# Performance work log

Measured on AMD Instinct MI355X. Metric: run time of the kernel, lower is better.

Reference implementation:

```python
import jax, jax.numpy as jnp
import numpy as np

E = 8        # num_experts
D = 512      # embed_size
H = 8        # attention heads
HD = D // H  # head dim
B, S = 4, 1024


def setup_inputs() -> dict:
    key = jax.random.key(0)
    ks = jax.random.split(key, 16)
    sd = 0.02
    return {
        "x":  jax.random.normal(ks[0], (B, S, D), jnp.float32),
        # per-expert FFN params, stacked over expert dim
        "W1": jax.random.normal(ks[1], (E, D, 4 * D), jnp.float32) * sd,
        "b1": jnp.zeros((E, 4 * D), jnp.float32),
        "W2": jax.random.normal(ks[2], (E, 4 * D, D), jnp.float32) * sd,
        "b2": jnp.zeros((E, D), jnp.float32),
        # MultiheadAttention in_proj (split) and out_proj
        "Wq": jax.random.normal(ks[3], (D, D), jnp.float32) * sd,
        "bq": jnp.zeros((D,), jnp.float32),
        "Wk": jax.random.normal(ks[4], (D, D), jnp.float32) * sd,
        "bk": jnp.zeros((D,), jnp.float32),
        "Wv": jax.random.normal(ks[5], (D, D), jnp.float32) * sd,
        "bv": jnp.zeros((D,), jnp.float32),
        "Wo": jax.random.normal(ks[6], (D, D), jnp.float32) * sd,
        "bo": jnp.zeros((D,), jnp.float32),
        "expert_id": 3,
    }


def reference(x, W1, b1, W2, b2, Wq, bq, Wk, bk, Wv, bv, Wo, bo, expert_id):
    # --- batched per-expert FFN (fuses the Python loop over experts) ---
    # hidden: [B, E, S, 4D]
    hidden = jax.nn.relu(jnp.einsum('bsd,edf->besf', x, W1) + b1[None, :, None, :])
    eo = jnp.einsum('besf,efd->besd', hidden, W2) + b2[None, :, None, :]  # [B,E,S,D]
    eo = eo.transpose(0, 2, 1, 3)  # [B, S, E, D]

    Bs, Ss = x.shape[0], x.shape[1]
    a = eo.reshape(Bs * Ss, E, D)  # [N, E, D]; attention runs over the expert dim

    # --- MultiheadAttention (batch_first), torch semantics ---
    # NOTE: the original passes a FLOAT tril-of-ones attn_mask, which torch ADDS
    # to the scores (it does NOT mask with -inf). We reproduce that faithfully.
    q = (a @ Wq.T + bq).reshape(-1, E, H, HD).transpose(0, 2, 1, 3)  # [N,H,E,hd]
    k = (a @ Wk.T + bk).reshape(-1, E, H, HD).transpose(0, 2, 1, 3)
    v = (a @ Wv.T + bv).reshape(-1, E, H, HD).transpose(0, 2, 1, 3)

    mask = jnp.tril(jnp.ones((E, E), jnp.float32))  # additive float mask
    scores = jnp.einsum('nhed,nhfd->nhef', q, k) / jnp.sqrt(jnp.float32(HD))
    scores = scores + mask[None, None, :, :]
    attn = jax.nn.softmax(scores, axis=-1)
    ctx = jnp.einsum('nhef,nhfd->nhed', attn, v)           # [N,H,E,hd]
    ctx = ctx.transpose(0, 2, 1, 3).reshape(-1, E, D)       # [N,E,D]
    out = ctx @ Wo.T + bo                                   # [N,E,D]

    out = out.reshape(Bs, Ss, E, D)
    return out[:, :, expert_id, :]  # [B, S, D]
```

## Files before the change

### kernel.cpp

```cpp
#include <hip/hip_runtime.h>
#include <hip/hip_bf16.h>

typedef __hip_bfloat16 bf16;
typedef __attribute__((ext_vector_type(4))) float f32x4;
typedef __attribute__((ext_vector_type(8))) short s16x8;

#define N_TOK 4096
#define Dm    512
#define Fm    2048
#define Em    8

__device__ __forceinline__ float bf2f(bf16 v) { return __bfloat162float(v); }
__device__ __forceinline__ bf16  f2bf(float f) { return __float2bfloat16(f); }

#define GL16(g, l)                                                              \
  __builtin_amdgcn_global_load_lds(                                             \
      (const __attribute__((address_space(1))) void*)(g),                       \
      (__attribute__((address_space(3))) void*)(l), 16, 0, 0)

__global__ void cvt_f32_bf16(const float* __restrict__ in, bf16* __restrict__ out, int n4) {
  int i = blockIdx.x * 256 + threadIdx.x;
  if (i >= n4) return;
  float4 v = reinterpret_cast<const float4*>(in)[i];
  bf16 tmp[4] = {f2bf(v.x), f2bf(v.y), f2bf(v.z), f2bf(v.w)};
  __builtin_memcpy(out + (size_t)i * 4, tmp, 8);
}

__global__ void transpose_cvt(const float* __restrict__ in, bf16* __restrict__ out,
                              int R, int C, long inb, long outb) {
  in  += (long)blockIdx.z * inb;
  out += (long)blockIdx.z * outb;
  __shared__ float t[32][33];
  int tx = threadIdx.x & 31, ty = threadIdx.x >> 5;
  int c0 = blockIdx.x * 32, r0 = blockIdx.y * 32;
#pragma unroll
  for (int i = 0; i < 32; i += 8)
    t[ty + i][tx] = in[(long)(r0 + ty + i) * C + c0 + tx];
  __syncthreads();
#pragma unroll
  for (int i = 0; i < 32; i += 8)
    out[(long)(c0 + ty + i) * R + r0 + tx] = f2bf(t[tx][ty + i]);
}

template <bool RELU, bool OUT_BF16>
__global__ __launch_bounds__(256, 4) void gemm128(
    const bf16* __restrict__ A, const bf16* __restrict__ Bt, void* __restrict__ Cout,
    const float* __restrict__ bias, int K, int lda, int ldb, int ldc,
    long abs_, long bbs, long cbs, long biasbs,
    const int* __restrict__ eid, int eid_scale) {
  __shared__ bf16 As[128 * 64];
  __shared__ bf16 Bs[128 * 64];

  int e  = blockIdx.z;
  int bm = blockIdx.x * 128, bn = blockIdx.y * 128;

  A    += (long)e * abs_;
  Bt   += (long)e * bbs;
  bias += (long)e * biasbs;
  long coff = (long)e * cbs;
  if (eid) A += (long)(*eid) * eid_scale;

  int tid = threadIdx.x, wv = tid >> 6, lane = tid & 63;
  int wm = wv >> 1, wn = wv & 1;

  const bf16* Ab = A + (long)bm * lda;
  const bf16* Bb = Bt + (long)bn * ldb;

  f32x4 acc[4][4] = {};
  int la = lane & 15, q = lane >> 4;
  int srow_lo = lane >> 3;

  for (int k0 = 0; k0 < K; k0 += 64) {
    __syncthreads();
#pragma unroll
    for (int j = 0; j < 4; ++j) {
      int r = (wv * 4 + j) * 8 + srow_lo;
      int c = (lane & 7) ^ (r & 7);
      GL16(Ab + (long)r * lda + k0 + c * 8, As + (wv * 4 + j) * 512);
      GL16(Bb + (long)r * ldb + k0 + c * 8, Bs + (wv * 4 + j) * 512);
    }
    __syncthreads();

#pragma unroll
    for (int kk = 0; kk < 2; ++kk) {
      int ps = (kk * 4 + q) ^ (la & 7);
      s16x8 af[4], bfr[4];
#pragma unroll
      for (int m = 0; m < 4; ++m)
        af[m] = *reinterpret_cast<const s16x8*>(As + (wm * 64 + m * 16 + la) * 64 + ps * 8);
#pragma unroll
      for (int n = 0; n < 4; ++n)
        bfr[n] = *reinterpret_cast<const s16x8*>(Bs + (wn * 64 + n * 16 + la) * 64 + ps * 8);
#pragma unroll
      for (int m = 0; m < 4; ++m)
#pragma unroll
        for (int n = 0; n < 4; ++n)
          acc[m][n] = __builtin_amdgcn_mfma_f32_16x16x32_bf16(bfr[n], af[m], acc[m][n], 0, 0, 0);
    }
  }

#pragma unroll
  for (int m = 0; m < 4; ++m) {
    int gm = bm + wm * 64 + m * 16 + la;
#pragma unroll
    for (int n = 0; n < 4; ++n) {
      int gn = bn + wn * 64 + n * 16 + q * 4;
      float4 b4 = *reinterpret_cast<const float4*>(bias + gn);
      float v0 = acc[m][n][0] + b4.x, v1 = acc[m][n][1] + b4.y;
      float v2 = acc[m][n][2] + b4.z, v3 = acc[m][n][3] + b4.w;
      if (RELU) {
        v0 = fmaxf(v0, 0.f); v1 = fmaxf(v1, 0.f);
        v2 = fmaxf(v2, 0.f); v3 = fmaxf(v3, 0.f);
      }
      long idx = coff + (long)gm * ldc + gn;
      if (OUT_BF16) {
        bf16 tmp[4] = {f2bf(v0), f2bf(v1), f2bf(v2), f2bf(v3)};
        __builtin_memcpy((bf16*)Cout + idx, tmp, 8);
      } else {
        float tmp[4] = {v0, v1, v2, v3};
        __builtin_memcpy((float*)Cout + idx, tmp, 16);
      }
    }
  }
}

template <bool RELU, bool OUT_BF16>
__global__ __launch_bounds__(256, 2) void gemm_bt(
    const bf16* __restrict__ A, const bf16* __restrict__ Bt, void* __restrict__ Cout,
    const float* __restrict__ bias, int M, int N, int K, int lda, int ldb, int ldc,
    long abs_, long bbs, long cbs, long biasbs, const int* __restrict__ eid,
    int eid_scale) {
  int e = blockIdx.z;
  A    += (long)e * abs_;
  Bt   += (long)e * bbs;
  bias += (long)e * biasbs;
  long coff = (long)e * cbs;
  if (eid) A += (long)(*eid) * eid_scale;

  __shared__ bf16 As[128 * 32];
  __shared__ bf16 Bs[128 * 32];

  int tid = threadIdx.x;
  int wave = tid >> 6, lane = tid & 63;
  int wm = wave >> 1, wn = wave & 1;
  int bm = blockIdx.x * 128, bn = blockIdx.y * 128;

  int srow  = lane >> 2;
  int skoff = (lane & 3) * 8;

  f32x4 acc[4][4] = {};

  const bf16* Abase = A + (long)bm * lda;
  const bf16* Bbase = Bt + (long)bn * ldb;

  for (int k0 = 0; k0 < K; k0 += 32) {
    __syncthreads();
#pragma unroll
    for (int i = 0; i < 2; i++) {
      int r = wave * 32 + i * 16 + srow;
      GL16(Abase + (long)r * lda + k0 + skoff, As + (wave * 32 + i * 16) * 32);
      GL16(Bbase + (long)r * ldb + k0 + skoff, Bs + (wave * 32 + i * 16) * 32);
    }
    __syncthreads();

    s16x8 af[4], bfr[4];
#pragma unroll
    for (int m = 0; m < 4; m++)
      af[m] = *reinterpret_cast<const s16x8*>(As + (wm * 64 + m * 16 + (lane & 15)) * 32 +
                                              (lane >> 4) * 8);
#pragma unroll
    for (int n = 0; n < 4; n++)
      bfr[n] = *reinterpret_cast<const s16x8*>(Bs + (wn * 64 + n * 16 + (lane & 15)) * 32 +
                                               (lane >> 4) * 8);
#pragma unroll
    for (int m = 0; m < 4; m++)
#pragma unroll
      for (int n = 0; n < 4; n++)
        acc[m][n] = __builtin_amdgcn_mfma_f32_16x16x32_bf16(af[m], bfr[n], acc[m][n], 0, 0, 0);
  }

  int cr = (lane >> 4) * 4, cc = lane & 15;
#pragma unroll
  for (int m = 0; m < 4; m++) {
#pragma unroll
    for (int n = 0; n < 4; n++) {
      int col  = bn + wn * 64 + n * 16 + cc;
      float bv = bias ? bias[col] : 0.0f;
#pragma unroll
      for (int r = 0; r < 4; r++) {
        int row = bm + wm * 64 + m * 16 + cr + r;
        float v = acc[m][n][r] + bv;
        if (RELU) v = fmaxf(v, 0.0f);
        long idx = coff + (long)row * ldc + col;
        if (OUT_BF16)
          ((bf16*)Cout)[idx] = f2bf(v);
        else
          ((float*)Cout)[idx] = v;
      }
    }
  }
}

__global__ __launch_bounds__(256) void attn_kernel(const float* __restrict__ q,
                                                   const bf16* __restrict__ kv,
                                                   bf16* __restrict__ ctx,
                                                   const int* __restrict__ eid) {
  int wave = threadIdx.x >> 6, lane = threadIdx.x & 63;
  int n = blockIdx.x * 4 + wave;
  int h = lane >> 3, f = lane & 7;
  int e3 = *eid;
  const bf16* kvn = kv + (long)n * Em * (2 * Dm);
  const float* qh = q + (long)n * Dm + h * 64;
  const bf16* kf = kvn + f * (2 * Dm) + h * 64;
  float s = 0.f;
#pragma unroll
  for (int j = 0; j < 64; j++) s += qh[j] * bf2f(kf[j]);
  s *= 0.125f;
  s += (f <= e3) ? 1.0f : 0.0f;
  float mx = s;
#pragma unroll
  for (int d = 1; d < 8; d <<= 1) mx = fmaxf(mx, __shfl_xor(mx, d));
  float ex = expf(s - mx);
  float sm = ex;
#pragma unroll
  for (int d = 1; d < 8; d <<= 1) sm += __shfl_xor(sm, d);
  float at = ex / sm;
  int g = f;
  float acc[8] = {0, 0, 0, 0, 0, 0, 0, 0};
#pragma unroll
  for (int f2 = 0; f2 < 8; f2++) {
    float a = __shfl(at, (h << 3) | f2);
    const bf16* vf = kvn + f2 * (2 * Dm) + Dm + h * 64 + g * 8;
#pragma unroll
    for (int j = 0; j < 8; j++) acc[j] += a * bf2f(vf[j]);
  }
  bf16 tmp[8];
#pragma unroll
  for (int j = 0; j < 8; j++) tmp[j] = f2bf(acc[j]);
  __builtin_memcpy(ctx + (long)n * Dm + h * 64 + g * 8, tmp, 16);
}

extern "C" void kernel_launch(void* const* d_in, const int* in_sizes, int n_in,
                              void* d_out, int out_size, void* d_ws, size_t ws_size,
                              hipStream_t stream) {
  const float* x  = (const float*)d_in[0];
  const float* W1 = (const float*)d_in[1];
  const float* b1 = (const float*)d_in[2];
  const float* W2 = (const float*)d_in[3];
  const float* b2 = (const float*)d_in[4];
  const float* Wq = (const float*)d_in[5];
  const float* bq = (const float*)d_in[6];
  const float* Wk = (const float*)d_in[7];
  const float* bk = (const float*)d_in[8];
  const float* Wv = (const float*)d_in[9];
  const float* bv = (const float*)d_in[10];
  const float* Wo = (const float*)d_in[11];
  const float* bo = (const float*)d_in[12];
  const int* eid  = (const int*)d_in[13];

  char* w = (char*)d_ws;
  auto alloc = [&](size_t bytes) {
    char* p = w;
    w += (bytes + 255) & ~(size_t)255;
    return p;
  };
  bf16* xb   = (bf16*)alloc((size_t)N_TOK * Dm * 2);
  bf16* W1t  = (bf16*)alloc((size_t)Em * Fm * Dm * 2);
  bf16* W2t  = (bf16*)alloc((size_t)Em * Dm * Fm * 2);
  bf16* qw   = (bf16*)alloc((size_t)Dm * Dm * 2);
  bf16* kvw  = (bf16*)alloc((size_t)2 * Dm * Dm * 2);
  bf16* ow   = (bf16*)alloc((size_t)Dm * Dm * 2);
  float* bkv = (float*)alloc((size_t)2 * Dm * 4);
  bf16* hid  = (bf16*)alloc((size_t)Em * N_TOK * Fm * 2);
  bf16* eo   = (bf16*)alloc((size_t)N_TOK * Em * Dm * 2);
  bf16* kv   = (bf16*)hid;
  float* qb  = (float*)(hid + (size_t)N_TOK * Em * 2 * Dm);
  bf16* ctxb = (bf16*)(qb + (size_t)N_TOK * Dm);

  cvt_f32_bf16<<<(N_TOK * Dm / 4 + 255) / 256, 256, 0, stream>>>(x, xb, N_TOK * Dm / 4);
  transpose_cvt<<<dim3(Fm / 32, Dm / 32, Em), 256, 0, stream>>>(
      W1, W1t, Dm, Fm, (long)Dm * Fm, (long)Fm * Dm);
  transpose_cvt<<<dim3(Dm / 32, Fm / 32, Em), 256, 0, stream>>>(
      W2, W2t, Fm, Dm, (long)Fm * Dm, (long)Dm * Fm);
  int nw4 = Dm * Dm / 4;
  cvt_f32_bf16<<<(nw4 + 255) / 256, 256, 0, stream>>>(Wq, qw, nw4);
  cvt_f32_bf16<<<(nw4 + 255) / 256, 256, 0, stream>>>(Wk, kvw, nw4);
  cvt_f32_bf16<<<(nw4 + 255) / 256, 256, 0, stream>>>(Wv, kvw + (size_t)Dm * Dm, nw4);
  cvt_f32_bf16<<<(nw4 + 255) / 256, 256, 0, stream>>>(Wo, ow, nw4);
  hipMemcpyAsync(bkv, bk, Dm * sizeof(float), hipMemcpyDeviceToDevice, stream);
  hipMemcpyAsync(bkv + Dm, bv, Dm * sizeof(float), hipMemcpyDeviceToDevice, stream);

  gemm128<true, true><<<dim3(32, 16, Em), 256, 0, stream>>>(
      xb, W1t, hid, b1, Dm, Dm, Dm, Fm,
      0L, (long)Fm * Dm, (long)N_TOK * Fm, (long)Fm, nullptr, 0);
  gemm128<false, true><<<dim3(32, 4, Em), 256, 0, stream>>>(
      hid, W2t, eo, b2, Fm, Fm, Fm, Em * Dm,
      (long)N_TOK * Fm, (long)Dm * Fm, (long)Dm, (long)Dm, nullptr, 0);
  gemm128<false, true><<<dim3(256, 8, 1), 256, 0, stream>>>(
      eo, kvw, kv, bkv, Dm, Dm, Dm, 2 * Dm,
      0L, 0L, 0L, 0L, nullptr, 0);
  gemm_bt<false, false><<<dim3(N_TOK / 128, Dm / 128, 1), 256, 0, stream>>>(
      eo, qw, qb, bq, N_TOK, Dm, Dm, Em * Dm, Dm, Dm,
      0L, 0L, 0L, 0L, eid, Dm);
  attn_kernel<<<N_TOK / 4, 256, 0, stream>>>(qb, kv, ctxb, eid);
  gemm_bt<false, false><<<dim3(N_TOK / 128, Dm / 128, 1), 256, 0, stream>>>(
      ctxb, ow, (float*)d_out, bo, N_TOK, Dm, Dm, Dm, Dm, Dm,
      0L, 0L, 0L, 0L, nullptr, 0);
}
```

Before: 310.5 us.

## Replace LDS-staged GEMMs with direct global-to-register double-buffered MFMA GEMM

Drops the shared-memory staging (global_load_lds plus two barriers per k-step) and instead has each wave load its MFMA fragments straight from global memory into registers, using a two-stage register double buffer to overlap loads with MFMAs. The separate gemm_bt kernel is removed and all six GEMM launches go through the one new kernel. This removes LDS traffic and barriers, but gives up the sharing of data across waves, so each A/B fragment is fetched from global or L2 once per wave. The loads are 16-byte strided row reads that lean on cache hits.

```diff
diff --git a/kernel.cpp b/kernel.cpp
--- a/kernel.cpp
+++ b/kernel.cpp
@@ -12,11 +12,6 @@
 
 __device__ __forceinline__ float bf2f(bf16 v) { return __bfloat162float(v); }
 __device__ __forceinline__ bf16  f2bf(float f) { return __float2bfloat16(f); }
-
-#define GL16(g, l)                                                              \
-  __builtin_amdgcn_global_load_lds(                                             \
-      (const __attribute__((address_space(1))) void*)(g),                       \
-      (__attribute__((address_space(3))) void*)(l), 16, 0, 0)
 
 __global__ void cvt_f32_bf16(const float* __restrict__ in, bf16* __restrict__ out, int n4) {
   int i = blockIdx.x * 256 + threadIdx.x;
@@ -43,60 +38,61 @@
 }
 
 template <bool RELU, bool OUT_BF16>
-__global__ __launch_bounds__(256, 4) void gemm128(
+__global__ __launch_bounds__(256) void gemm_direct(
     const bf16* __restrict__ A, const bf16* __restrict__ Bt, void* __restrict__ Cout,
     const float* __restrict__ bias, int K, int lda, int ldb, int ldc,
     long abs_, long bbs, long cbs, long biasbs,
     const int* __restrict__ eid, int eid_scale) {
-  __shared__ bf16 As[128 * 64];
-  __shared__ bf16 Bs[128 * 64];
-
   int e  = blockIdx.z;
-  int bm = blockIdx.x * 128, bn = blockIdx.y * 128;
-
   A    += (long)e * abs_;
   Bt   += (long)e * bbs;
   bias += (long)e * biasbs;
   long coff = (long)e * cbs;
   if (eid) A += (long)(*eid) * eid_scale;
 
+  int bm = blockIdx.x * 128, bn = blockIdx.y * 128;
   int tid = threadIdx.x, wv = tid >> 6, lane = tid & 63;
   int wm = wv >> 1, wn = wv & 1;
-
-  const bf16* Ab = A + (long)bm * lda;
-  const bf16* Bb = Bt + (long)bn * ldb;
+  int la = lane & 15, q = lane >> 4;
+
+  const bf16* Ar[4];
+  const bf16* Br[4];
+#pragma unroll
+  for (int m = 0; m < 4; ++m)
+    Ar[m] = A + (long)(bm + wm * 64 + m * 16 + la) * lda + q * 8;
+#pragma unroll
+  for (int n = 0; n < 4; ++n)
+    Br[n] = Bt + (long)(bn + wn * 64 + n * 16 + la) * ldb + q * 8;
 
   f32x4 acc[4][4] = {};
-  int la = lane & 15, q = lane >> 4;
-  int srow_lo = lane >> 3;
+  s16x8 a0[4], b0[4], a1[4], b1[4];
+
+#pragma unroll
+  for (int m = 0; m < 4; ++m) a0[m] = *reinterpret_cast<const s16x8*>(Ar[m]);
+#pragma unroll
+  for (int n = 0; n < 4; ++n) b0[n] = *reinterpret_cast<const s16x8*>(Br[n]);
 
   for (int k0 = 0; k0 < K; k0 += 64) {
-    __syncthreads();
-#pragma unroll
-    for (int j = 0; j < 4; ++j) {
-      int r = (wv * 4 + j) * 8 + srow_lo;
-      int c = (lane & 7) ^ (r & 7);
-      GL16(Ab + (long)r * lda + k0 + c * 8, As + (wv * 4 + j) * 512);
-      GL16(Bb + (long)r * ldb + k0 + c * 8, Bs + (wv * 4 + j) * 512);
-    }
-    __syncthreads();
-
-#pragma unroll
-    for (int kk = 0; kk < 2; ++kk) {
-      int ps = (kk * 4 + q) ^ (la & 7);
-      s16x8 af[4], bfr[4];
-#pragma unroll
-      for (int m = 0; m < 4; ++m)
-        af[m] = *reinterpret_cast<const s16x8*>(As + (wm * 64 + m * 16 + la) * 64 + ps * 8);
+    int k1 = k0 + 32;
+    int k2 = (k0 + 64 < K) ? (k0 + 64) : (K - 32);
+#pragma unroll
+    for (int m = 0; m < 4; ++m) a1[m] = *reinterpret_cast<const s16x8*>(Ar[m] + k1);
+#pragma unroll
+    for (int n = 0; n < 4; ++n) b1[n] = *reinterpret_cast<const s16x8*>(Br[n] + k1);
+#pragma unroll
+    for (int m = 0; m < 4; ++m)
 #pragma unroll
       for (int n = 0; n < 4; ++n)
-        bfr[n] = *reinterpret_cast<const s16x8*>(Bs + (wn * 64 + n * 16 + la) * 64 + ps * 8);
-#pragma unroll
-      for (int m = 0; m < 4; ++m)
-#pragma unroll
-        for (int n = 0; n < 4; ++n)
-          acc[m][n] = __builtin_amdgcn_mfma_f32_16x16x32_bf16(bfr[n], af[m], acc[m][n], 0, 0, 0);
-    }
+        acc[m][n] = __builtin_amdgcn_mfma_f32_16x16x32_bf16(b0[n], a0[m], acc[m][n], 0, 0, 0);
+#pragma unroll
+    for (int m = 0; m < 4; ++m) a0[m] = *reinterpret_cast<const s16x8*>(Ar[m] + k2);
+#pragma unroll
+    for (int n = 0; n < 4; ++n) b0[n] = *reinterpret_cast<const s16x8*>(Br[n] + k2);
+#pragma unroll
+    for (int m = 0; m < 4; ++m)
+#pragma unroll
+      for (int n = 0; n < 4; ++n)
+        acc[m][n] = __builtin_amdgcn_mfma_f32_16x16x32_bf16(b1[n], a1[m], acc[m][n], 0, 0, 0);
   }
 
 #pragma unroll
@@ -124,83 +120,6 @@
   }
 }
 
-template <bool RELU, bool OUT_BF16>
-__global__ __launch_bounds__(256, 2) void gemm_bt(
-    const bf16* __restrict__ A, const bf16* __restrict__ Bt, void* __restrict__ Cout,
-    const float* __restrict__ bias, int M, int N, int K, int lda, int ldb, int ldc,
-    long abs_, long bbs, long cbs, long biasbs, const int* __restrict__ eid,
-    int eid_scale) {
-  int e = blockIdx.z;
-  A    += (long)e * abs_;
-  Bt   += (long)e * bbs;
-  bias += (long)e * biasbs;
-  long coff = (long)e * cbs;
-  if (eid) A += (long)(*eid) * eid_scale;
-
-  __shared__ bf16 As[128 * 32];
-  __shared__ bf16 Bs[128 * 32];
-
-  int tid = threadIdx.x;
-  int wave = tid >> 6, lane = tid & 63;
-  int wm = wave >> 1, wn = wave & 1;
-  int bm = blockIdx.x * 128, bn = blockIdx.y * 128;
-
-  int srow  = lane >> 2;
-  int skoff = (lane & 3) * 8;
-
-  f32x4 acc[4][4] = {};
-
-  const bf16* Abase = A + (long)bm * lda;
-  const bf16* Bbase = Bt + (long)bn * ldb;
-
-  for (int k0 = 0; k0 < K; k0 += 32) {
-    __syncthreads();
-#pragma unroll
-    for (int i = 0; i < 2; i++) {
-      int r = wave * 32 + i * 16 + srow;
-      GL16(Abase + (long)r * lda + k0 + skoff, As + (wave * 32 + i * 16) * 32);
-      GL16(Bbase + (long)r * ldb + k0 + skoff, Bs + (wave * 32 + i * 16) * 32);
-    }
-    __syncthreads();
-
-    s16x8 af[4], bfr[4];
-#pragma unroll
-    for (int m = 0; m < 4; m++)
-      af[m] = *reinterpret_cast<const s16x8*>(As + (wm * 64 + m * 16 + (lane & 15)) * 32 +
-                                              (lane >> 4) * 8);
-#pragma unroll
-    for (int n = 0; n < 4; n++)
-      bfr[n] = *reinterpret_cast<const s16x8*>(Bs + (wn * 64 + n * 16 + (lane & 15)) * 32 +
-                                               (lane >> 4) * 8);
-#pragma unroll
-    for (int m = 0; m < 4; m++)
-#pragma unroll
-      for (int n = 0; n < 4; n++)
-        acc[m][n] = __builtin_amdgcn_mfma_f32_16x16x32_bf16(af[m], bfr[n], acc[m][n], 0, 0, 0);
-  }
-
-  int cr = (lane >> 4) * 4, cc = lane & 15;
-#pragma unroll
-  for (int m = 0; m < 4; m++) {
-#pragma unroll
-    for (int n = 0; n < 4; n++) {
-      int col  = bn + wn * 64 + n * 16 + cc;
-      float bv = bias ? bias[col] : 0.0f;
-#pragma unroll
-      for (int r = 0; r < 4; r++) {
-        int row = bm + wm * 64 + m * 16 + cr + r;
-        float v = acc[m][n][r] + bv;
-        if (RELU) v = fmaxf(v, 0.0f);
-        long idx = coff + (long)row * ldc + col;
-        if (OUT_BF16)
-          ((bf16*)Cout)[idx] = f2bf(v);
-        else
-          ((float*)Cout)[idx] = v;
-      }
-    }
-  }
-}
-
 __global__ __launch_bounds__(256) void attn_kernel(const float* __restrict__ q,
                                                    const bf16* __restrict__ kv,
                                                    bf16* __restrict__ ctx,
@@ -290,20 +209,20 @@
   hipMemcpyAsync(bkv, bk, Dm * sizeof(float), hipMemcpyDeviceToDevice, stream);
   hipMemcpyAsync(bkv + Dm, bv, Dm * sizeof(float), hipMemcpyDeviceToDevice, stream);
 
-  gemm128<true, true><<<dim3(32, 16, Em), 256, 0, stream>>>(
+  gemm_direct<true, true><<<dim3(32, 16, Em), 256, 0, stream>>>(
       xb, W1t, hid, b1, Dm, Dm, Dm, Fm,
       0L, (long)Fm * Dm, (long)N_TOK * Fm, (long)Fm, nullptr, 0);
-  gemm128<false, true><<<dim3(32, 4, Em), 256, 0, stream>>>(
+  gemm_direct<false, true><<<dim3(32, 4, Em), 256, 0, stream>>>(
       hid, W2t, eo, b2, Fm, Fm, Fm, Em * Dm,
       (long)N_TOK * Fm, (long)Dm * Fm, (long)Dm, (long)Dm, nullptr, 0);
-  gemm128<false, true><<<dim3(256, 8, 1), 256, 0, stream>>>(
+  gemm_direct<false, true><<<dim3(256, 8, 1), 256, 0, stream>>>(
       eo, kvw, kv, bkv, Dm, Dm, Dm, 2 * Dm,
       0L, 0L, 0L, 0L, nullptr, 0);
-  gemm_bt<false, false><<<dim3(N_TOK / 128, Dm / 128, 1), 256, 0, stream>>>(
-      eo, qw, qb, bq, N_TOK, Dm, Dm, Em * Dm, Dm, Dm,
+  gemm_direct<false, false><<<dim3(32, 4, 1), 256, 0, stream>>>(
+      eo, qw, qb, bq, Dm, Em * Dm, Dm, Dm,
       0L, 0L, 0L, 0L, eid, Dm);
   attn_kernel<<<N_TOK / 4, 256, 0, stream>>>(qb, kv, ctxb, eid);
-  gemm_bt<false, false><<<dim3(N_TOK / 128, Dm / 128, 1), 256, 0, stream>>>(
-      ctxb, ow, (float*)d_out, bo, N_TOK, Dm, Dm, Dm, Dm, Dm,
+  gemm_direct<false, false><<<dim3(32, 4, 1), 256, 0, stream>>>(
+      ctxb, ow, (float*)d_out, bo, Dm, Dm, Dm, Dm,
       0L, 0L, 0L, 0L, nullptr, 0);
 }
```

New measurement: 742.5 us. 2.39x slower.
